# Performance work log

Measured on AMD Instinct MI355X. Metric: run time of the kernel, lower is better.

Reference implementation:

```python
import jax, jax.numpy as jnp
import numpy as np

N = 10000      # nodes
E = 160000     # edges (avg degree 16)
D = 480        # node feat dim: 128x0e+64x1e+32x2e
SH = 9         # spherical harmonics dim, lmax=2, component norm
NB = 128       # radial basis count
H = 4          # attention heads
HD = D // H    # 120 = 32x0e+16x1o+8x2e
L = 6          # transformer blocks
G = 256        # graphs in batch
MID = 480      # ffn mid dim (irreps_mlp_mid)
S = 128        # scalar (0e) channels used by the output head
FCH = 64       # radial MLP hidden (fc_neurons)
CUTOFF = 5.0
AVG_DEG = 16.0
AVG_NODES = 18.0


def _sph_l2(vec):
    # real spherical harmonics l=0,1,2 on normalized vectors, 'component' normalization
    r = jnp.linalg.norm(vec, axis=-1, keepdims=True)
    u = vec / (r + 1e-9)
    x, y, z = u[..., 0], u[..., 1], u[..., 2]
    s3, s15, s5 = jnp.sqrt(3.0), jnp.sqrt(15.0), jnp.sqrt(5.0)
    return jnp.stack([
        jnp.ones_like(x),
        s3 * x, s3 * y, s3 * z,
        s15 * x * y, s15 * y * z, 0.5 * s5 * (3.0 * z * z - 1.0),
        s15 * x * z, 0.5 * s15 * (x * x - y * y)], axis=-1)


def _rbf(d):
    centers = jnp.linspace(0.0, CUTOFF, NB)
    w = CUTOFF / NB
    return jnp.exp(-0.5 * ((d[:, None] - centers) / w) ** 2)  # [E, NB]


def _ln(x):
    mu = jnp.mean(x, axis=-1, keepdims=True)
    var = jnp.var(x, axis=-1, keepdims=True)
    return (x - mu) * jax.lax.rsqrt(var + 1e-5)


def _radial_mlp(rb, w1, w2, w3):
    h = jax.nn.silu(rb @ w1)
    h = jax.nn.silu(h @ w2)
    return h @ w3


def _segment_softmax(logits, seg, num_segments):
    m = jax.ops.segment_max(logits, seg, num_segments=num_segments)
    ex = jnp.exp(logits - m[seg])
    s = jax.ops.segment_sum(ex, seg, num_segments=num_segments)
    return ex / (s[seg] + 1e-9)


def setup_inputs():
    key = jax.random.key(0)
    ks = jax.random.split(key, 24)
    def rn(k, shape, scale):
        return jax.random.normal(k, shape, dtype=jnp.float32) * scale
    return {
        'z': jax.random.randint(ks[0], (N,), 0, 100),
        'pos': jax.random.normal(ks[1], (N, 3), dtype=jnp.float32) * 3.0,
        'batch': jnp.sort(jax.random.randint(ks[2], (N,), 0, G)),
        'edge_src': jax.random.randint(ks[3], (E,), 0, N),
        'edge_dst': jax.random.randint(ks[4], (E,), 0, N),
        'atom_emb': rn(ks[5], (100, D), 1.0),
        'W_deg_sh': rn(ks[6], (SH, D), SH ** -0.5),
        'deg_w1': rn(ks[7], (NB, FCH), NB ** -0.5),
        'deg_w2': rn(ks[8], (FCH, FCH), FCH ** -0.5),
        'deg_w3': rn(ks[9], (FCH, D), FCH ** -0.5),
        'Wv': rn(ks[10], (L, D, D), D ** -0.5),
        'Wsh': rn(ks[11], (L, SH, D), SH ** -0.5),
        'rad_w1': rn(ks[12], (L, NB, FCH), NB ** -0.5),
        'rad_w2': rn(ks[13], (L, FCH, FCH), FCH ** -0.5),
        'rad_w3': rn(ks[14], (L, FCH, D), FCH ** -0.5),
        'attn_a': rn(ks[15], (L, H, HD), HD ** -0.5),
        'Wo': rn(ks[16], (L, D, D), D ** -0.5),
        'ffn_w1': rn(ks[17], (L, D, MID), D ** -0.5),
        'ffn_w2': rn(ks[18], (L, MID, D), MID ** -0.5),
        'head_w1': rn(ks[19], (S, S), S ** -0.5),
        'head_w2': rn(ks[20], (S, S), S ** -0.5),
    }


def reference(z, pos, batch, edge_src, edge_dst, atom_emb, W_deg_sh,
              deg_w1, deg_w2, deg_w3, Wv, Wsh, rad_w1, rad_w2, rad_w3,
              attn_a, Wo, ffn_w1, ffn_w2, head_w1, head_w2):
    # edge geometry features
    vec = pos[edge_src] - pos[edge_dst]                      # [E, 3]
    sh = _sph_l2(vec)                                        # [E, SH]
    rb = _rbf(jnp.linalg.norm(vec, axis=-1))                 # [E, NB]

    # node embedding + edge-degree embedding (scatter to dst, scaled by avg degree)
    emb = atom_emb[z]                                        # [N, D]
    deg_gate = _radial_mlp(rb, deg_w1, deg_w2, deg_w3)       # [E, D]
    deg = jax.ops.segment_sum((sh @ W_deg_sh) * deg_gate, edge_dst,
                              num_segments=N) / AVG_DEG
    x = emb + deg

    # equivariant tensor-product attention blocks (gather -> per-edge TP -> segment softmax -> scatter)
    for l in range(L):
        xn = _ln(x)
        v = xn[edge_src] @ Wv[l]                             # [E, D] gather + proj
        msg = v * (sh @ Wsh[l]) * _radial_mlp(rb, rad_w1[l], rad_w2[l], rad_w3[l])
        m = msg.reshape(E, H, HD)
        logits = jnp.einsum('ehd,hd->eh', jax.nn.leaky_relu(m, 0.2), attn_a[l])
        alpha = _segment_softmax(logits, edge_dst, N)        # [E, H]
        agg = jax.ops.segment_sum(m * alpha[:, :, None], edge_dst,
                                  num_segments=N).reshape(N, D)
        x = x + agg @ Wo[l]
        x = x + jax.nn.silu(_ln(x) @ ffn_w1[l]) @ ffn_w2[l]

    # output head on scalar channels, scaled scatter over molecules
    s = _ln(x[:, :S])
    h = jax.nn.silu(s @ head_w1) @ head_w2                   # [N, S]
    out = jax.ops.segment_sum(h, batch, num_segments=G) / jnp.sqrt(AVG_NODES)
    return out
```

## Files before the change

kernel.cpp:

```cpp
#include <hip/hip_runtime.h>
#include <hip/hip_bf16.h>
#include <math.h>

#define NN 10000
#define NE 160000
#define DIM 480
#define NSH 9
#define NBASIS 128
#define NHEAD 4
#define HDIM 120
#define NL 6
#define NG 256
#define NS 128
#define FCH 64
#define CUTOFF 5.0f
#define NEB 2500

typedef __attribute__((ext_vector_type(8))) short bf8v;
typedef __attribute__((ext_vector_type(4))) float f4v;

__device__ __forceinline__ float silu_f(float v) { return v / (1.0f + __expf(-v)); }
__device__ __forceinline__ float bf2f(ushort u) { return __uint_as_float(((unsigned)u) << 16); }
__device__ __forceinline__ ushort f2bfu(float f) {
  __hip_bfloat16 h = __float2bfloat16(f);
  return *reinterpret_cast<ushort*>(&h);
}

__device__ __forceinline__ void nt_store16(char* dst, uint4 v) {
  unsigned* p = (unsigned*)dst;
  __builtin_nontemporal_store(v.x, p + 0);
  __builtin_nontemporal_store(v.y, p + 1);
  __builtin_nontemporal_store(v.z, p + 2);
  __builtin_nontemporal_store(v.w, p + 3);
}
__device__ __forceinline__ uint4 nt_load16(const char* src) {
  const unsigned* p = (const unsigned*)src;
  uint4 v;
  v.x = __builtin_nontemporal_load(p + 0);
  v.y = __builtin_nontemporal_load(p + 1);
  v.z = __builtin_nontemporal_load(p + 2);
  v.w = __builtin_nontemporal_load(p + 3);
  return v;
}

struct bf16x4 { __hip_bfloat16 v[4]; };

__global__ void k_zero_int(int* p, int n)
{
  int i = blockIdx.x * 256 + threadIdx.x;
  if (i < n) p[i] = 0;
}

__global__ void k_count(const int* __restrict__ edst, int* __restrict__ cnt)
{
  int e = blockIdx.x * 256 + threadIdx.x;
  if (e < NE) atomicAdd(&cnt[edst[e]], 1);
}

__global__ __launch_bounds__(1024)
void k_scan(const int* __restrict__ cnt, int* __restrict__ row_ptr)
{
  __shared__ int part[1024];
  int tid = threadIdx.x;
  const int per = 10;
  int base = tid * per;
  int s = 0;
  for (int i = 0; i < per; i++) { int idx = base + i; if (idx < NN) s += cnt[idx]; }
  part[tid] = s; __syncthreads();
  for (int off = 1; off < 1024; off <<= 1) {
    int v = (tid >= off) ? part[tid - off] : 0;
    __syncthreads();
    part[tid] += v;
    __syncthreads();
  }
  int run = (tid > 0) ? part[tid - 1] : 0;
  for (int i = 0; i < per; i++) {
    int idx = base + i;
    if (idx < NN) { row_ptr[idx] = run; run += cnt[idx]; }
  }
  if (tid == 1023) row_ptr[NN] = part[1023];
}

__global__ void k_fill(const int* __restrict__ edst, const int* __restrict__ row_ptr,
                       int* __restrict__ cursor, int* __restrict__ csr)
{
  int e = blockIdx.x * 256 + threadIdx.x;
  if (e >= NE) return;
  int d = edst[e];
  int p = atomicAdd(&cursor[d], 1);
  csr[row_ptr[d] + p] = e;
}

__global__ void k_geom_p(const float* __restrict__ pos, const int* __restrict__ esrc,
                         const int* __restrict__ edst, const int* __restrict__ csr,
                         __hip_bfloat16* __restrict__ shb, float* __restrict__ distp,
                         int* __restrict__ esrcp, int* __restrict__ edstp)
{
  int j = blockIdx.x * 256 + threadIdx.x;
  if (j >= NE) return;
  int e = csr[j];
  int s = esrc[e], d = edst[e];
  esrcp[j] = s;
  edstp[j] = d;
  float vx = pos[s*3+0] - pos[d*3+0];
  float vy = pos[s*3+1] - pos[d*3+1];
  float vz = pos[s*3+2] - pos[d*3+2];
  float r = sqrtf(vx*vx + vy*vy + vz*vz);
  distp[j] = r;
  float inv = 1.0f / (r + 1e-9f);
  float x = vx*inv, y = vy*inv, z = vz*inv;
  const float s3 = 1.7320508075688772f;
  const float s15 = 3.872983346207417f;
  const float s5 = 2.23606797749979f;
  float sv[9];
  sv[0] = 1.0f;
  sv[1] = s3*x; sv[2] = s3*y; sv[3] = s3*z;
  sv[4] = s15*x*y; sv[5] = s15*y*z; sv[6] = 0.5f*s5*(3.0f*z*z - 1.0f);
  sv[7] = s15*x*z; sv[8] = 0.5f*s15*(x*x - y*y);
  __hip_bfloat16* o = shb + (size_t)j * 16;
#pragma unroll
  for (int q = 0; q < 9; q++) o[q] = __float2bfloat16(sv[q]);
#pragma unroll
  for (int q = 9; q < 16; q++) o[q] = __float2bfloat16(0.f);
}

__global__ void k_prep(const float* __restrict__ deg_w3, const float* __restrict__ rad_w3,
                       const float* __restrict__ W_deg_sh, const float* __restrict__ Wsh,
                       __hip_bfloat16* __restrict__ w3T, __hip_bfloat16* __restrict__ wshT)
{
  int i = blockIdx.x * 256 + threadIdx.x;
  if (i < 7*512*64) {
    int l = i / (512*64); int r = i - l*512*64; int col = r >> 6; int k = r & 63;
    float v = 0.f;
    if (col < DIM) {
      const float* src = (l == 0) ? deg_w3 : rad_w3 + (size_t)(l-1)*FCH*DIM;
      v = src[k*DIM + col];
    }
    w3T[i] = __float2bfloat16(v);
  }
  int j = i - 7*512*64;
  if (j >= 0 && j < 7*512*32) {
    int l = j / (512*32); int r = j - l*512*32; int col = r >> 5; int q = r & 31;
    float v = 0.f;
    if (col < DIM && q < 9) {
      const float* src = (l == 0) ? W_deg_sh : Wsh + (size_t)(l-1)*NSH*DIM;
      v = src[q*DIM + col];
    }
    wshT[j] = __float2bfloat16(v);
  }
}

__global__ void k_prepw(const float* __restrict__ Wv, const float* __restrict__ Wo,
                        const float* __restrict__ f1, const float* __restrict__ f2,
                        const float* __restrict__ h1, const float* __restrict__ h2w,
                        __hip_bfloat16* __restrict__ WT)
{
  int i = blockIdx.x * 256 + threadIdx.x;
  const int big = 24*512*480;
  if (i < big) {
    int m = i / (512*480); int r = i - m*(512*480); int col = r / 480; int k = r - col*480;
    int l = m % 6; int t = m / 6;
    const float* src = (t==0 ? Wv : t==1 ? Wo : t==2 ? f1 : f2) + (size_t)l*DIM*DIM;
    float v = (col < DIM) ? src[k*DIM + col] : 0.f;
    WT[i] = __float2bfloat16(v);
  } else if (i < big + 2*128*128) {
    int j = i - big; int m = j / (128*128); int r = j - m*(128*128);
    int col = r >> 7; int k = r & 127;
    const float* src = m ? h2w : h1;
    WT[i] = __float2bfloat16(src[k*128 + col]);
  }
}

__global__ __launch_bounds__(256)
void k_radial(const float* __restrict__ dist, const float* __restrict__ w1,
              const float* __restrict__ w2, __hip_bfloat16* __restrict__ h2out)
{
  __shared__ float rbs[NBASIS][65];
  __shared__ float wsm[NBASIS * FCH];
  __shared__ float ds[64];
  int tid = threadIdx.x;
  int e0 = blockIdx.x * 64;
  if (tid < 64) ds[tid] = dist[e0 + tid];
  for (int i = tid; i < NBASIS * FCH; i += 256) wsm[i] = w1[i];
  __syncthreads();
  const float invw = (float)NBASIS / CUTOFF;
  for (int i = tid; i < NBASIS * 64; i += 256) {
    int k = i >> 6, e = i & 63;
    float c = k * (CUTOFF / 127.0f);
    float tt = (ds[e] - c) * invw;
    rbs[k][e] = __expf(-0.5f * tt * tt);
  }
  __syncthreads();
  int ty = tid >> 4, tx = tid & 15;
  float acc1[4][4] = {};
  for (int k = 0; k < NBASIS; k++) {
    float b[4];
#pragma unroll
    for (int j = 0; j < 4; j++) b[j] = wsm[k*FCH + tx*4 + j];
#pragma unroll
    for (int i = 0; i < 4; i++) {
      float a = rbs[k][ty*4 + i];
#pragma unroll
      for (int j = 0; j < 4; j++) acc1[i][j] = fmaf(a, b[j], acc1[i][j]);
    }
  }
  __syncthreads();
#pragma unroll
  for (int i = 0; i < 4; i++)
#pragma unroll
    for (int j = 0; j < 4; j++)
      rbs[tx*4 + j][ty*4 + i] = silu_f(acc1[i][j]);
  for (int i = tid; i < FCH * FCH; i += 256) wsm[i] = w2[i];
  __syncthreads();
  float acc2[4][4] = {};
  for (int k = 0; k < FCH; k++) {
    float b[4];
#pragma unroll
    for (int j = 0; j < 4; j++) b[j] = wsm[k*FCH + tx*4 + j];
#pragma unroll
    for (int i = 0; i < 4; i++) {
      float a = rbs[k][ty*4 + i];
#pragma unroll
      for (int j = 0; j < 4; j++) acc2[i][j] = fmaf(a, b[j], acc2[i][j]);
    }
  }
#pragma unroll
  for (int i = 0; i < 4; i++) {
    int e = e0 + ty*4 + i;
    bf16x4 p;
#pragma unroll
    for (int j = 0; j < 4; j++) p.v[j] = __float2bfloat16(silu_f(acc2[i][j]));
    *(bf16x4*)(h2out + (size_t)e*FCH + tx*4) = p;
  }
}

__global__ __launch_bounds__(256)
void k_stats(const float* __restrict__ in, float* __restrict__ st,
             int n, int cols, int stride)
{
  int row = blockIdx.x * 4 + (threadIdx.x >> 6);
  int lane = threadIdx.x & 63;
  if (row >= n) return;
  const float* r = in + (size_t)row * stride;
  float s = 0.f, ss = 0.f;
  for (int c = lane; c < cols; c += 64) { float v = r[c]; s += v; ss += v*v; }
  for (int off = 32; off > 0; off >>= 1) { s += __shfl_down(s, off); ss += __shfl_down(ss, off); }
  if (lane == 0) {
    float mu = s / cols;
    float var = ss / cols - mu * mu;
    st[row*2]   = mu;
    st[row*2+1] = rsqrtf(fmaxf(var, 0.f) + 1e-5f);
  }
}

template<int ADD, int SILU, int LNA, int OBF16>
__global__ __launch_bounds__(256)
void k_gemmm(const float* __restrict__ A, const __hip_bfloat16* __restrict__ BT,
             float* __restrict__ C, __hip_bfloat16* __restrict__ Cb,
             const float* __restrict__ st, int M, int K, int Nc, int lda)
{
  __shared__ __align__(16) char smA[4096];
  __shared__ __align__(16) char smB[8192];
  __shared__ float smu[64], srs[64];
  int tid = threadIdx.x;
  int lane = tid & 63;
  int wv = tid >> 6;
  int l15 = lane & 15, l4 = lane >> 4;
  int row0 = blockIdx.x * 64;
  int col0 = blockIdx.y * 128;
  if (LNA && tid < 64) {
    int gr = row0 + tid;
    float m2 = 0.f, r2 = 1.f;
    if (gr < M) { m2 = st[gr*2]; r2 = st[gr*2+1]; }
    smu[tid] = m2; srs[tid] = r2;
  }
  f4v z4 = {0.f,0.f,0.f,0.f};
  f4v acc[8];
#pragma unroll
  for (int ct = 0; ct < 8; ct++) acc[ct] = z4;

  int arow = tid >> 2, aq = tid & 3;
  int bcol = tid >> 1, bh = tid & 1;
  for (int k0 = 0; k0 < K; k0 += 32) {
    __syncthreads();
    {
      int grow = row0 + arow;
      float f[8];
      if (grow < M) {
        const float* ap = A + (size_t)grow * lda + k0 + aq*8;
        float4 v0 = *(const float4*)ap;
        float4 v1 = *(const float4*)(ap + 4);
        f[0]=v0.x; f[1]=v0.y; f[2]=v0.z; f[3]=v0.w;
        f[4]=v1.x; f[5]=v1.y; f[6]=v1.z; f[7]=v1.w;
      } else {
#pragma unroll
        for (int q = 0; q < 8; q++) f[q] = 0.f;
      }
      if (LNA) {
        float mu = smu[arow], rs = srs[arow];
#pragma unroll
        for (int q = 0; q < 8; q++) f[q] = (f[q] - mu) * rs;
      }
      unsigned u[4];
#pragma unroll
      for (int q = 0; q < 4; q++)
        u[q] = (unsigned)f2bfu(f[2*q]) | ((unsigned)f2bfu(f[2*q+1]) << 16);
      int base = arow*64 + aq*16;
      *(uint4*)(smA + (base ^ ((arow&7)<<4))) = make_uint4(u[0],u[1],u[2],u[3]);
    }
    {
      const ushort* bp = (const ushort*)BT + (size_t)(col0 + bcol) * K + k0 + bh*16;
      uint4 v0 = *(const uint4*)bp;
      uint4 v1 = *(const uint4*)(bp + 8);
      int base = bcol*64 + bh*32;
      *(uint4*)(smB + (base ^ ((bcol&7)<<4))) = v0;
      *(uint4*)(smB + ((base+16) ^ ((bcol&7)<<4))) = v1;
    }
    __syncthreads();
    int r0 = wv*16 + l15;
    bf8v a0 = *(const bf8v*)(smA + ((r0*64 + l4*16) ^ ((r0&7)<<4)));
#pragma unroll
    for (int ct = 0; ct < 8; ct++) {
      int cc = ct*16 + l15;
      bf8v b = *(const bf8v*)(smB + ((cc*64 + l4*16) ^ ((cc&7)<<4)));
      acc[ct] = __builtin_amdgcn_mfma_f32_16x16x32_bf16(a0, b, acc[ct], 0, 0, 0);
    }
  }
#pragma unroll
  for (int ct = 0; ct < 8; ct++)
#pragma unroll
  for (int e = 0; e < 4; e++) {
    int row = row0 + wv*16 + l4*4 + e;
    int col = col0 + ct*16 + l15;
    if (row < M && col < Nc) {
      float v = acc[ct][e];
      if (SILU) v = silu_f(v);
      if (OBF16) Cb[(size_t)row * Nc + col] = __float2bfloat16(v);
      else {
        float* p = C + (size_t)row * Nc + col;
        if (ADD) *p += v; else *p = v;
      }
    }
  }
}

template<int MODE, int STOREM>
__global__ __launch_bounds__(256)
void k_msgm(const __hip_bfloat16* __restrict__ h2, const __hip_bfloat16* __restrict__ shb,
            const int* __restrict__ esrcp, const int* __restrict__ edstp,
            const __hip_bfloat16* __restrict__ w3T, const __hip_bfloat16* __restrict__ wshT,
            const float* __restrict__ aa, const __hip_bfloat16* __restrict__ y,
            const float* __restrict__ alpha, float* __restrict__ outbuf,
            float* __restrict__ logits, __hip_bfloat16* __restrict__ msgb)
{
  __shared__ __align__(16) char sm_h2[8192];
  __shared__ __align__(16) char sm_w3[16384];
  __shared__ __align__(16) char sm_sh[4096];
  __shared__ __align__(16) char sm_wsh[8192];
  __shared__ int srcs[(MODE<=1)?64:1];
  __shared__ int dsts[(MODE>=1)?64:1];
  __shared__ int segidL[(MODE>=1)?64:1];
  __shared__ int seg_dstL[(MODE>=1)?32:1];

  int bid = blockIdx.x;
  int xcd = bid & 7;
  const int qq = NEB >> 3, rr = NEB & 7;
  int basee = (xcd < rr) ? xcd * (qq + 1) : rr * (qq + 1) + (xcd - rr) * qq;
  int eblk = basee + (bid >> 3);
  int e0 = eblk * 64;

  int tid = threadIdx.x;
  int lane = tid & 63;
  int wv = tid >> 6;
  int l15 = lane & 15, l4 = lane >> 4;
  int wrow0 = wv * 16;

  for (int c = tid; c < 512; c += 256) {
    int r = c >> 3, s = c & 7;
    uint4 v = *(const uint4*)((const char*)h2 + (size_t)(e0 + r) * 128 + s * 16);
    *(uint4*)(sm_h2 + ((r * 128 + s * 16) ^ ((r & 7) << 4))) = v;
  }
  {
    int r = tid >> 2, q = tid & 3;
    uint4 v = make_uint4(0u, 0u, 0u, 0u);
    if (q < 2)
      v = *(const uint4*)((const ushort*)shb + (size_t)(e0 + r) * 16 + q * 8);
    *(uint4*)(sm_sh + ((r * 64 + q * 16) ^ ((r & 7) << 4))) = v;
  }
  if (tid < 64) {
    if (MODE <= 1) srcs[tid] = esrcp[e0 + tid];
    if (MODE >= 1) dsts[tid] = edstp[e0 + tid];
  }
  __syncthreads();

  int nseg = 0;
  if (MODE >= 1) {
    if (tid < 64) {
      bool flag = (tid == 0) || (dsts[tid] != dsts[tid - 1]);
      unsigned long long m = __ballot(flag ? 1 : 0);
      unsigned long long below = m & (~0ull >> (63 - tid));
      int sg = __popcll(below) - 1;
      segidL[tid] = sg;
      if (flag && sg < 32) seg_dstL[sg] = dsts[tid];
    }
    __syncthreads();
    nseg = segidL[63] + 1;
  }

  int srcs4[4];
  float4 al4[4];
#pragma unroll
  for (int e = 0; e < 4; e++) {
    int rl = wrow0 + l4 * 4 + e;
    if (MODE <= 1) srcs4[e] = srcs[rl];
    if (MODE == 1) al4[e] = *(const float4*)(alpha + (size_t)(e0 + rl) * 4);
  }

  const ushort* yus = (const ushort*)y;
  f4v z4 = {0.f, 0.f, 0.f, 0.f};
  float lacc[4][4];
  if (MODE == 0) {
#pragma unroll
    for (int e = 0; e < 4; e++)
#pragma unroll
      for (int h = 0; h < 4; h++) lacc[e][h] = 0.f;
  }

#pragma unroll
  for (int ci = 0; ci < 4; ci++) {
    int col0 = ci * 128;
    __syncthreads();
    for (int c = tid; c < 1024; c += 256) {
      int r = c >> 3, s = c & 7;
      uint4 v = *(const uint4*)((const char*)w3T + (size_t)(col0 + r) * 128 + s * 16);
      *(uint4*)(sm_w3 + ((r * 128 + s * 16) ^ ((r & 7) << 4))) = v;
    }
    for (int c = tid; c < 512; c += 256) {
      int r = c >> 2, q = c & 3;
      uint4 v = *(const uint4*)((const ushort*)wshT + (size_t)(col0 + r) * 32 + q * 8);
      *(uint4*)(sm_wsh + ((r * 64 + q * 16) ^ ((r & 7) << 4))) = v;
    }
    __syncthreads();

    f4v g[8];
#pragma unroll
    for (int ct = 0; ct < 8; ct++) g[ct] = z4;

#pragma unroll
    for (int ks = 0; ks < 2; ks++) {
      int k0b = (ks * 32 + l4 * 8) * 2;
      int r0 = wrow0 + l15;
      bf8v a0 = *(const bf8v*)(sm_h2 + ((r0 * 128 + k0b) ^ ((r0 & 7) << 4)));
#pragma unroll
      for (int ct = 0; ct < 8; ct++) {
        int cc = ct * 16 + l15;
        bf8v b = *(const bf8v*)(sm_w3 + ((cc * 128 + k0b) ^ ((cc & 7) << 4)));
        g[ct] = __builtin_amdgcn_mfma_f32_16x16x32_bf16(a0, b, g[ct], 0, 0, 0);
      }
    }

    {
      int r0 = wrow0 + l15;
      bf8v shA = *(const bf8v*)(sm_sh + ((r0 * 64 + l4 * 16) ^ ((r0 & 7) << 4)));
#pragma unroll
      for (int ct = 0; ct < 8; ct++) {
        int cc = ct * 16 + l15;
        int col = col0 + cc;
        bf8v wB = *(const bf8v*)(sm_wsh + ((cc * 64 + l4 * 16) ^ ((cc & 7) << 4)));
        f4v sw4 = __builtin_amdgcn_mfma_f32_16x16x32_bf16(shA, wB, z4, 0, 0, 0);
#pragma unroll
        for (int e = 0; e < 4; e++) {
          float yv;
          if (MODE == 2) yv = 1.f;
          else yv = (col < DIM) ? bf2f(yus[(size_t)srcs4[e] * DIM + col]) : 0.f;
          float mv = yv * sw4[e] * g[ct][e];
          if (MODE == 1) {
            float av = (col < 120) ? al4[e].x : (col < 240) ? al4[e].y
                     : (col < 360) ? al4[e].z : al4[e].w;
            mv *= av;
          }
          if (MODE == 2) mv *= (1.0f / 16.0f);
          g[ct][e] = mv;
        }
      }
    }

    if (MODE == 0) {
      float aav[8];
#pragma unroll
      for (int ct = 0; ct < 8; ct++) {
        int col = col0 + ct * 16 + l15;
        aav[ct] = (col < DIM) ? aa[col] : 0.f;
      }
#pragma unroll
      for (int e = 0; e < 4; e++) {
        float sA = 0.f, sB = 0.f;
#pragma unroll
        for (int ct = 0; ct < 8; ct++) {
          int col = col0 + ct * 16 + l15;
          float mv = g[ct][e];
          float lv = (mv > 0.f) ? mv : 0.2f * mv;
          float c = lv * aav[ct];
          if (col / 120 == ci) sA += c; else sB += c;
        }
#pragma unroll
        for (int off = 1; off < 16; off <<= 1) {
          sA += __shfl_xor(sA, off, 16);
          sB += __shfl_xor(sB, off, 16);
        }
        lacc[e][ci] += sA;
        if (ci < 3) lacc[e][ci + 1] += sB;
      }
      if (STOREM) {
        __syncthreads();
#pragma unroll
        for (int ct = 0; ct < 8; ct++) {
          int cc = ct * 16 + l15;
          int ebase = wrow0 + l4 * 4;
          ushort4 pk;
          pk.x = f2bfu(g[ct][0]); pk.y = f2bfu(g[ct][1]);
          pk.z = f2bfu(g[ct][2]); pk.w = f2bfu(g[ct][3]);
          *(ushort4*)(sm_w3 + ((cc * 128 + ebase * 2) ^ ((cc & 7) << 4))) = pk;
        }
        __syncthreads();
        char* gdst = (char*)msgb + (size_t)(eblk * 4 + ci) * 16384;
#pragma unroll
        for (int k = 0; k < 4; k++) {
          int o = tid * 16 + k * 4096;
          uint4 v = *(const uint4*)(sm_w3 + o);
          nt_store16(gdst + o, v);
        }
      }
    } else if (nseg > 32) {
#pragma unroll
      for (int e = 0; e < 4; e++) {
        int rl = wrow0 + l4 * 4 + e;
        int dd = dsts[rl];
#pragma unroll
        for (int ct = 0; ct < 8; ct++) {
          int col = col0 + ct * 16 + l15;
          if (col < DIM) atomicAdd(&outbuf[(size_t)dd * DIM + col], g[ct][e]);
        }
      }
    } else {
      __syncthreads();
#pragma unroll
      for (int ct = 0; ct < 8; ct++) {
        int cc = ct * 16 + l15;
        int ebase = wrow0 + l4 * 4;
        ushort4 pk;
        pk.x = f2bfu(g[ct][0]); pk.y = f2bfu(g[ct][1]);
        pk.z = f2bfu(g[ct][2]); pk.w = f2bfu(g[ct][3]);
        *(ushort4*)(sm_w3 + ((cc * 128 + ebase * 2) ^ ((cc & 7) << 4))) = pk;
      }
      __syncthreads();
      f4v p[2][2];
      p[0][0] = z4; p[0][1] = z4; p[1][0] = z4; p[1][1] = z4;
#pragma unroll
      for (int ks = 0; ks < 2; ks++) {
        int k0 = ks * 32 + l4 * 8;
        bf8v a0, a1;
#pragma unroll
        for (int e2 = 0; e2 < 8; e2++) {
          int sg = segidL[k0 + e2];
          a0[e2] = (sg == l15)      ? (short)0x3F80 : (short)0;
          a1[e2] = (sg == l15 + 16) ? (short)0x3F80 : (short)0;
        }
#pragma unroll
        for (int c2 = 0; c2 < 2; c2++) {
          int cc = (wv * 2 + c2) * 16 + l15;
          bf8v bm = *(const bf8v*)(sm_w3 + ((cc * 128 + k0 * 2) ^ ((cc & 7) << 4)));
          p[0][c2] = __builtin_amdgcn_mfma_f32_16x16x32_bf16(a0, bm, p[0][c2], 0, 0, 0);
          p[1][c2] = __builtin_amdgcn_mfma_f32_16x16x32_bf16(a1, bm, p[1][c2], 0, 0, 0);
        }
      }
#pragma unroll
      for (int rt = 0; rt < 2; rt++)
#pragma unroll
      for (int c2 = 0; c2 < 2; c2++)
#pragma unroll
      for (int e = 0; e < 4; e++) {
        int seg = rt * 16 + l4 * 4 + e;
        int col = col0 + (wv * 2 + c2) * 16 + l15;
        if (seg < nseg && col < DIM) {
          float v = p[rt][c2][e];
          float* ptr = outbuf + (size_t)seg_dstL[seg] * DIM + col;
          if (seg == 0 || seg == nseg - 1) atomicAdd(ptr, v);
          else if (MODE == 1) *ptr = v;
          else *ptr += v;
        }
      }
    }
  }

  if (MODE == 0) {
#pragma unroll
    for (int e = 0; e < 4; e++) {
      int row = e0 + wrow0 + l4 * 4 + e;
      if (l15 == 0) {
        logits[(size_t)row * 4 + 0] = lacc[e][0];
        logits[(size_t)row * 4 + 1] = lacc[e][1];
        logits[(size_t)row * 4 + 2] = lacc[e][2];
        logits[(size_t)row * 4 + 3] = lacc[e][3];
      }
    }
  }
}

__global__ __launch_bounds__(256)
void k_aggm(const __hip_bfloat16* __restrict__ msgb, const int* __restrict__ edstp,
            const float* __restrict__ alpha, float* __restrict__ agg)
{
  __shared__ __align__(16) char smM[16384];
  __shared__ __align__(16) float alsq[64][4];
  __shared__ int dsts[64];
  __shared__ int segidL[64];
  __shared__ int seg_dstL[32];

  int bid = blockIdx.x;
  int swzb = (bid & 7) * 1250 + (bid >> 3);
  int e0   = (swzb >> 2) * 64;
  int col0 = (swzb & 3) * 128;
  int tid = threadIdx.x;
  int lane = tid & 63;
  int wv = tid >> 6;
  int l15 = lane & 15, l4 = lane >> 4;

  if (tid < 64) {
    dsts[tid] = edstp[e0 + tid];
    *(float4*)&alsq[tid][0] = *(const float4*)(alpha + (size_t)(e0 + tid) * 4);
  }
  __syncthreads();

  int nseg = 0;
  if (tid < 64) {
    bool flag = (tid == 0) || (dsts[tid] != dsts[tid - 1]);
    unsigned long long m = __ballot(flag ? 1 : 0);
    unsigned long long below = m & (~0ull >> (63 - tid));
    int sg = __popcll(below) - 1;
    segidL[tid] = sg;
    if (flag && sg < 32) seg_dstL[sg] = dsts[tid];
  }
  __syncthreads();
  nseg = segidL[63] + 1;

  const char* gsrc = (const char*)msgb + (size_t)swzb * 16384;
  uint4 vv[4];
#pragma unroll
  for (int k = 0; k < 4; k++) {
    int o = tid * 16 + k * 4096;
    uint4 v = nt_load16(gsrc + o);
    int cc = o >> 7;
    int col = col0 + cc;
    int h = (col < DIM) ? (col / 120) : 3;
    int be = ((o & 127) ^ ((cc & 7) << 4)) >> 1;
    unsigned w[4] = {v.x, v.y, v.z, v.w};
#pragma unroll
    for (int q = 0; q < 4; q++) {
      float lo = bf2f((ushort)(w[q] & 0xffffu)) * alsq[be + 2*q][h];
      float hi = bf2f((ushort)(w[q] >> 16))     * alsq[be + 2*q + 1][h];
      w[q] = (unsigned)f2bfu(lo) | ((unsigned)f2bfu(hi) << 16);
    }
    vv[k] = make_uint4(w[0], w[1], w[2], w[3]);
    *(uint4*)(smM + o) = vv[k];
  }
  __syncthreads();

  if (nseg > 32) {
#pragma unroll
    for (int k = 0; k < 4; k++) {
      int o = tid * 16 + k * 4096;
      int cc = o >> 7;
      int col = col0 + cc;
      if (col >= DIM) continue;
      int be = ((o & 127) ^ ((cc & 7) << 4)) >> 1;
      unsigned w[4] = {vv[k].x, vv[k].y, vv[k].z, vv[k].w};
#pragma unroll
      for (int q = 0; q < 4; q++) {
        atomicAdd(&agg[(size_t)dsts[be + 2*q]   * DIM + col], bf2f((ushort)(w[q] & 0xffffu)));
        atomicAdd(&agg[(size_t)dsts[be + 2*q+1] * DIM + col], bf2f((ushort)(w[q] >> 16)));
      }
    }
    return;
  }

  f4v z4 = {0.f,0.f,0.f,0.f};
  f4v p[2][2];
  p[0][0] = z4; p[0][1] = z4; p[1][0] = z4; p[1][1] = z4;
#pragma unroll
  for (int ks = 0; ks < 2; ks++) {
    int k0 = ks * 32 + l4 * 8;
    bf8v a0, a1;
#pragma unroll
    for (int e2 = 0; e2 < 8; e2++) {
      int sg = segidL[k0 + e2];
      a0[e2] = (sg == l15)      ? (short)0x3F80 : (short)0;
      a1[e2] = (sg == l15 + 16) ? (short)0x3F80 : (short)0;
    }
#pragma unroll
    for (int c2 = 0; c2 < 2; c2++) {
      int cc = (wv * 2 + c2) * 16 + l15;
      bf8v bm = *(const bf8v*)(smM + ((cc * 128 + k0 * 2) ^ ((cc & 7) << 4)));
      p[0][c2] = __builtin_amdgcn_mfma_f32_16x16x32_bf16(a0, bm, p[0][c2], 0, 0, 0);
      p[1][c2] = __builtin_amdgcn_mfma_f32_16x16x32_bf16(a1, bm, p[1][c2], 0, 0, 0);
    }
  }
#pragma unroll
  for (int rt = 0; rt < 2; rt++)
#pragma unroll
  for (int c2 = 0; c2 < 2; c2++)
#pragma unroll
  for (int e = 0; e < 4; e++) {
    int seg = rt * 16 + l4 * 4 + e;
    int col = col0 + (wv * 2 + c2) * 16 + l15;
    if (seg < nseg && col < DIM) {
      float v = p[rt][c2][e];
      float* ptr = agg + (size_t)seg_dstL[seg] * DIM + col;
      if (seg == 0 || seg == nseg - 1) atomicAdd(ptr, v);
      else *ptr = v;
    }
  }
}

__global__ void k_alpha(const int* __restrict__ row_ptr, const float* __restrict__ logits,
                        float* __restrict__ alpha)
{
  int i = blockIdx.x * 256 + threadIdx.x;
  if (i >= NN * NHEAD) return;
  int d = i >> 2, h = i & 3;
  int beg = row_ptr[d], end = row_ptr[d+1];
  if (beg == end) return;
  float m = -1e30f;
  for (int j = beg; j < end; j++) m = fmaxf(m, logits[(size_t)j*NHEAD + h]);
  float s = 0.f;
  for (int j = beg; j < end; j++) {
    float ex = __expf(logits[(size_t)j*NHEAD + h] - m);
    alpha[(size_t)j*NHEAD + h] = ex;
    s += ex;
  }
  float inv = 1.f / (s + 1e-9f);
  for (int j = beg; j < end; j++) alpha[(size_t)j*NHEAD + h] *= inv;
}

__global__ void k_init_x(const int* __restrict__ z, const float* __restrict__ emb,
                         float* __restrict__ x)
{
  int i = blockIdx.x * 256 + threadIdx.x;
  if (i >= NN * DIM) return;
  int n = i / DIM, c = i - n * DIM;
  x[i] = emb[(size_t)z[n]*DIM + c];
}

__global__ void k_scatter(const float* __restrict__ h, const int* __restrict__ batch,
                          float* __restrict__ out)
{
  int i = blockIdx.x * 256 + threadIdx.x;
  if (i >= NN * NS) return;
  int n = i >> 7;
  atomicAdd(&out[(size_t)batch[n]*NS + (i & 127)], h[i] * 0.23570226039551584f);
}

extern "C" void kernel_launch(void* const* d_in, const int* in_sizes, int n_in,
                              void* d_out, int out_size, void* d_ws, size_t ws_size,
                              hipStream_t stream)
{
  const int*   z        = (const int*)  d_in[0];
  const float* pos      = (const float*)d_in[1];
  const int*   batch    = (const int*)  d_in[2];
  const int*   esrc     = (const int*)  d_in[3];
  const int*   edst     = (const int*)  d_in[4];
  const float* atom_emb = (const float*)d_in[5];
  const float* W_deg_sh = (const float*)d_in[6];
  const float* deg_w1   = (const float*)d_in[7];
  const float* deg_w2   = (const float*)d_in[8];
  const float* deg_w3   = (const float*)d_in[9];
  const float* Wv       = (const float*)d_in[10];
  const float* Wsh      = (const float*)d_in[11];
  const float* rad_w1   = (const float*)d_in[12];
  const float* rad_w2   = (const float*)d_in[13];
  const float* rad_w3   = (const float*)d_in[14];
  const float* attn_a   = (const float*)d_in[15];
  const float* Wo       = (const float*)d_in[16];
  const float* ffn_w1   = (const float*)d_in[17];
  const float* ffn_w2   = (const float*)d_in[18];
  const float* head_w1  = (const float*)d_in[19];
  const float* head_w2  = (const float*)d_in[20];
  float* out = (float*)d_out;

  float* x      = (float*)d_ws;
  float* statsb = x      + (size_t)NN * DIM;
  float* agg    = statsb + (size_t)NN * 2;
  float* distp  = agg    + (size_t)NN * DIM;
  float* logitsb= distp  + (size_t)NE;
  float* alphab = logitsb+ (size_t)NE * NHEAD * 2;
  __hip_bfloat16* yb    = (__hip_bfloat16*)(alphab + (size_t)NE * NHEAD);
  __hip_bfloat16* h2b   = yb + (size_t)NN * DIM;
  __hip_bfloat16* shb16 = h2b + (size_t)NE * FCH;
  __hip_bfloat16* w3Tb  = shb16 + (size_t)NE * 16;
  __hip_bfloat16* wshTb = w3Tb + (size_t)7 * 512 * 64;
  __hip_bfloat16* bigWT = wshTb + (size_t)7 * 512 * 32;
  int* cnt      = (int*)(bigWT + (size_t)24*512*480 + 2*128*128);
  int* row_ptr  = cnt + NN;
  int* csr      = row_ptr + NN + 1;
  int* cursor   = csr + NE;
  int* esrcp    = cursor + NN;
  int* edstp    = esrcp + NE;
  __hip_bfloat16* msgb = (__hip_bfloat16*)(edstp + NE);
  float* tmp = logitsb;

  size_t needed = (size_t)((char*)msgb + (size_t)10000 * 16384 - (char*)d_ws);
  bool fast = ws_size >= needed;

  dim3 b256(256);
  k_zero_int<<<(NN+255)/256, b256, 0, stream>>>(cnt, NN);
  k_count<<<(NE+255)/256, b256, 0, stream>>>(edst, cnt);
  k_scan<<<1, 1024, 0, stream>>>(cnt, row_ptr);
  k_zero_int<<<(NN+255)/256, b256, 0, stream>>>(cursor, NN);
  k_fill<<<(NE+255)/256, b256, 0, stream>>>(edst, row_ptr, cursor, csr);
  k_geom_p<<<(NE+255)/256, b256, 0, stream>>>(pos, esrc, edst, csr, shb16, distp, esrcp, edstp);
  k_prep<<<(7*512*64 + 7*512*32 + 255)/256, b256, 0, stream>>>(deg_w3, rad_w3, W_deg_sh, Wsh,
      w3Tb, wshTb);
  k_prepw<<<(24*512*480 + 2*128*128 + 255)/256, b256, 0, stream>>>(Wv, Wo, ffn_w1, ffn_w2,
      head_w1, head_w2, bigWT);

  k_radial<<<NE/64, b256, 0, stream>>>(distp, deg_w1, deg_w2, h2b);
  k_init_x<<<(NN*DIM+255)/256, b256, 0, stream>>>(z, atom_emb, x);
  k_msgm<2,0><<<NEB, b256, 0, stream>>>(h2b, shb16, esrcp, edstp, w3Tb, wshTb,
      nullptr, nullptr, nullptr, x, nullptr, nullptr);

  dim3 gemm_grid(157, 4);
  dim3 head_grid(157, 1);
  for (int l = 0; l < NL; l++) {
    const float* w1_l  = rad_w1 + (size_t)l*NBASIS*FCH;
    const float* w2_l  = rad_w2 + (size_t)l*FCH*FCH;
    const float* aa_l  = attn_a + (size_t)l*NHEAD*HDIM;
    const __hip_bfloat16* w3T_l  = w3Tb  + (size_t)(l+1)*512*64;
    const __hip_bfloat16* wshT_l = wshTb + (size_t)(l+1)*512*32;
    const __hip_bfloat16* WvT_l = bigWT + (size_t)(0+l)*512*480;
    const __hip_bfloat16* WoT_l = bigWT + (size_t)(6+l)*512*480;
    const __hip_bfloat16* F1T_l = bigWT + (size_t)(12+l)*512*480;
    const __hip_bfloat16* F2T_l = bigWT + (size_t)(18+l)*512*480;

    k_stats<<<(NN+3)/4, b256, 0, stream>>>(x, statsb, NN, DIM, DIM);
    k_gemmm<0,0,1,1><<<gemm_grid, b256, 0, stream>>>(x, WvT_l, nullptr, yb, statsb,
        NN, DIM, DIM, DIM);
    k_radial<<<NE/64, b256, 0, stream>>>(distp, w1_l, w2_l, h2b);
    if (fast) {
      k_msgm<0,1><<<NEB, b256, 0, stream>>>(h2b, shb16, esrcp, edstp, w3T_l, wshT_l,
          aa_l, yb, nullptr, nullptr, logitsb, msgb);
      k_alpha<<<(NN*NHEAD+255)/256, b256, 0, stream>>>(row_ptr, logitsb, alphab);
      hipMemsetAsync(agg, 0, (size_t)NN * DIM * sizeof(float), stream);
      k_aggm<<<10000, b256, 0, stream>>>(msgb, edstp, alphab, agg);
    } else {
      k_msgm<0,0><<<NEB, b256, 0, stream>>>(h2b, shb16, esrcp, edstp, w3T_l, wshT_l,
          aa_l, yb, nullptr, nullptr, logitsb, nullptr);
      k_alpha<<<(NN*NHEAD+255)/256, b256, 0, stream>>>(row_ptr, logitsb, alphab);
      hipMemsetAsync(agg, 0, (size_t)NN * DIM * sizeof(float), stream);
      k_msgm<1,0><<<NEB, b256, 0, stream>>>(h2b, shb16, esrcp, edstp, w3T_l, wshT_l,
          nullptr, yb, alphab, agg, nullptr, nullptr);
    }
    k_gemmm<1,0,0,0><<<gemm_grid, b256, 0, stream>>>(agg, WoT_l, x, nullptr, nullptr,
        NN, DIM, DIM, DIM);
    k_stats<<<(NN+3)/4, b256, 0, stream>>>(x, statsb, NN, DIM, DIM);
    k_gemmm<0,1,1,0><<<gemm_grid, b256, 0, stream>>>(x, F1T_l, agg, nullptr, statsb,
        NN, DIM, DIM, DIM);
    k_gemmm<1,0,0,0><<<gemm_grid, b256, 0, stream>>>(agg, F2T_l, x, nullptr, nullptr,
        NN, DIM, DIM, DIM);
  }

  const __hip_bfloat16* H1T = bigWT + (size_t)24*512*480;
  const __hip_bfloat16* H2T = H1T + 128*128;
  k_stats<<<(NN+3)/4, b256, 0, stream>>>(x, statsb, NN, NS, DIM);
  k_gemmm<0,1,1,0><<<head_grid, b256, 0, stream>>>(x, H1T, agg, nullptr, statsb,
      NN, NS, NS, DIM);
  k_gemmm<0,0,0,0><<<head_grid, b256, 0, stream>>>(agg, H2T, tmp, nullptr, nullptr,
      NN, NS, NS, NS);
  hipMemsetAsync(d_out, 0, (size_t)NG * NS * sizeof(float), stream);
  k_scatter<<<(NN*NS+255)/256, b256, 0, stream>>>(tmp, batch, out);
}
```

Measured before the change: 2.377 ms.

## Fuse layernorm stats into residual GEMM epilogue and loop aggm over column tiles

The residual-add GEMMs now accumulate per-row sum and sum-of-squares via shuffles and atomics into a stats buffer, and a tiny finalize kernel replaces the separate k_stats pass that reread x. The aggregation kernel now processes all four column tiles of an edge block in one workgroup (2500 blocks instead of 10000) with a balanced XCD mapping, reusing destination/segment setup and alpha loads. This adds atomics and extra memsets per layer, and single-pass variance in fp32 with atomic ordering may change numerics slightly.

```diff
diff --git a/kernel.cpp b/kernel.cpp
--- a/kernel.cpp
+++ b/kernel.cpp
@@ -253,11 +253,23 @@
   }
 }
 
-template<int ADD, int SILU, int LNA, int OBF16>
+__global__ void k_finstat(const float* __restrict__ stacc, float* __restrict__ st, int n)
+{
+  int row = blockIdx.x * 256 + threadIdx.x;
+  if (row >= n) return;
+  float s = stacc[row*2], ss = stacc[row*2+1];
+  float mu = s / DIM;
+  float var = ss / DIM - mu * mu;
+  st[row*2]   = mu;
+  st[row*2+1] = rsqrtf(fmaxf(var, 0.f) + 1e-5f);
+}
+
+template<int ADD, int SILU, int LNA, int OBF16, int STATS>
 __global__ __launch_bounds__(256)
 void k_gemmm(const float* __restrict__ A, const __hip_bfloat16* __restrict__ BT,
              float* __restrict__ C, __hip_bfloat16* __restrict__ Cb,
-             const float* __restrict__ st, int M, int K, int Nc, int lda)
+             const float* __restrict__ st, int M, int K, int Nc, int lda,
+             float* __restrict__ stacc)
 {
   __shared__ __align__(16) char smA[4096];
   __shared__ __align__(16) char smB[8192];
@@ -327,18 +339,33 @@
     }
   }
 #pragma unroll
-  for (int ct = 0; ct < 8; ct++)
-#pragma unroll
   for (int e = 0; e < 4; e++) {
     int row = row0 + wv*16 + l4*4 + e;
-    int col = col0 + ct*16 + l15;
-    if (row < M && col < Nc) {
-      float v = acc[ct][e];
-      if (SILU) v = silu_f(v);
-      if (OBF16) Cb[(size_t)row * Nc + col] = __float2bfloat16(v);
-      else {
-        float* p = C + (size_t)row * Nc + col;
-        if (ADD) *p += v; else *p = v;
+    float s = 0.f, ss = 0.f;
+#pragma unroll
+    for (int ct = 0; ct < 8; ct++) {
+      int col = col0 + ct*16 + l15;
+      if (row < M && col < Nc) {
+        float v = acc[ct][e];
+        if (SILU) v = silu_f(v);
+        if (OBF16) Cb[(size_t)row * Nc + col] = __float2bfloat16(v);
+        else {
+          float* p = C + (size_t)row * Nc + col;
+          float xn = ADD ? (*p + v) : v;
+          *p = xn;
+          if (STATS) { s += xn; ss += xn * xn; }
+        }
+      }
+    }
+    if (STATS) {
+#pragma unroll
+      for (int off = 1; off < 16; off <<= 1) {
+        s  += __shfl_xor(s,  off, 16);
+        ss += __shfl_xor(ss, off, 16);
+      }
+      if (l15 == 0 && row < M) {
+        atomicAdd(&stacc[row*2],   s);
+        atomicAdd(&stacc[row*2+1], ss);
       }
     }
   }
@@ -618,9 +645,12 @@
   __shared__ int seg_dstL[32];
 
   int bid = blockIdx.x;
-  int swzb = (bid & 7) * 1250 + (bid >> 3);
-  int e0   = (swzb >> 2) * 64;
-  int col0 = (swzb & 3) * 128;
+  int xcd = bid & 7;
+  const int qq = NEB >> 3, rr = NEB & 7;
+  int basee = (xcd < rr) ? xcd * (qq + 1) : rr * (qq + 1) + (xcd - rr) * qq;
+  int eblk = basee + (bid >> 3);
+  int e0 = eblk * 64;
+
   int tid = threadIdx.x;
   int lane = tid & 63;
   int wv = tid >> 6;
@@ -644,80 +674,85 @@
   __syncthreads();
   nseg = segidL[63] + 1;
 
-  const char* gsrc = (const char*)msgb + (size_t)swzb * 16384;
-  uint4 vv[4];
-#pragma unroll
-  for (int k = 0; k < 4; k++) {
-    int o = tid * 16 + k * 4096;
-    uint4 v = nt_load16(gsrc + o);
-    int cc = o >> 7;
-    int col = col0 + cc;
-    int h = (col < DIM) ? (col / 120) : 3;
-    int be = ((o & 127) ^ ((cc & 7) << 4)) >> 1;
-    unsigned w[4] = {v.x, v.y, v.z, v.w};
-#pragma unroll
-    for (int q = 0; q < 4; q++) {
-      float lo = bf2f((ushort)(w[q] & 0xffffu)) * alsq[be + 2*q][h];
-      float hi = bf2f((ushort)(w[q] >> 16))     * alsq[be + 2*q + 1][h];
-      w[q] = (unsigned)f2bfu(lo) | ((unsigned)f2bfu(hi) << 16);
-    }
-    vv[k] = make_uint4(w[0], w[1], w[2], w[3]);
-    *(uint4*)(smM + o) = vv[k];
-  }
-  __syncthreads();
-
-  if (nseg > 32) {
+  f4v z4 = {0.f,0.f,0.f,0.f};
+#pragma unroll
+  for (int ci = 0; ci < 4; ci++) {
+    int col0 = ci * 128;
+    __syncthreads();
+    const char* gsrc = (const char*)msgb + (size_t)(eblk * 4 + ci) * 16384;
+    uint4 vv[4];
 #pragma unroll
     for (int k = 0; k < 4; k++) {
       int o = tid * 16 + k * 4096;
+      uint4 v = nt_load16(gsrc + o);
       int cc = o >> 7;
       int col = col0 + cc;
-      if (col >= DIM) continue;
+      int h = (col < DIM) ? (col / 120) : 3;
       int be = ((o & 127) ^ ((cc & 7) << 4)) >> 1;
-      unsigned w[4] = {vv[k].x, vv[k].y, vv[k].z, vv[k].w};
+      unsigned w[4] = {v.x, v.y, v.z, v.w};
 #pragma unroll
       for (int q = 0; q < 4; q++) {
-        atomicAdd(&agg[(size_t)dsts[be + 2*q]   * DIM + col], bf2f((ushort)(w[q] & 0xffffu)));
-        atomicAdd(&agg[(size_t)dsts[be + 2*q+1] * DIM + col], bf2f((ushort)(w[q] >> 16)));
-      }
-    }
-    return;
-  }
-
-  f4v z4 = {0.f,0.f,0.f,0.f};
-  f4v p[2][2];
-  p[0][0] = z4; p[0][1] = z4; p[1][0] = z4; p[1][1] = z4;
-#pragma unroll
-  for (int ks = 0; ks < 2; ks++) {
-    int k0 = ks * 32 + l4 * 8;
-    bf8v a0, a1;
-#pragma unroll
-    for (int e2 = 0; e2 < 8; e2++) {
-      int sg = segidL[k0 + e2];
-      a0[e2] = (sg == l15)      ? (short)0x3F80 : (short)0;
-      a1[e2] = (sg == l15 + 16) ? (short)0x3F80 : (short)0;
-    }
-#pragma unroll
-    for (int c2 = 0; c2 < 2; c2++) {
-      int cc = (wv * 2 + c2) * 16 + l15;
-      bf8v bm = *(const bf8v*)(smM + ((cc * 128 + k0 * 2) ^ ((cc & 7) << 4)));
-      p[0][c2] = __builtin_amdgcn_mfma_f32_16x16x32_bf16(a0, bm, p[0][c2], 0, 0, 0);
-      p[1][c2] = __builtin_amdgcn_mfma_f32_16x16x32_bf16(a1, bm, p[1][c2], 0, 0, 0);
-    }
-  }
-#pragma unroll
-  for (int rt = 0; rt < 2; rt++)
-#pragma unroll
-  for (int c2 = 0; c2 < 2; c2++)
-#pragma unroll
-  for (int e = 0; e < 4; e++) {
-    int seg = rt * 16 + l4 * 4 + e;
-    int col = col0 + (wv * 2 + c2) * 16 + l15;
-    if (seg < nseg && col < DIM) {
-      float v = p[rt][c2][e];
-      float* ptr = agg + (size_t)seg_dstL[seg] * DIM + col;
-      if (seg == 0 || seg == nseg - 1) atomicAdd(ptr, v);
-      else *ptr = v;
+        float lo = bf2f((ushort)(w[q] & 0xffffu)) * alsq[be + 2*q][h];
+        float hi = bf2f((ushort)(w[q] >> 16))     * alsq[be + 2*q + 1][h];
+        w[q] = (unsigned)f2bfu(lo) | ((unsigned)f2bfu(hi) << 16);
+      }
+      vv[k] = make_uint4(w[0], w[1], w[2], w[3]);
+      *(uint4*)(smM + o) = vv[k];
+    }
+    __syncthreads();
+
+    if (nseg > 32) {
+#pragma unroll
+      for (int k = 0; k < 4; k++) {
+        int o = tid * 16 + k * 4096;
+        int cc = o >> 7;
+        int col = col0 + cc;
+        if (col >= DIM) continue;
+        int be = ((o & 127) ^ ((cc & 7) << 4)) >> 1;
+        unsigned w[4] = {vv[k].x, vv[k].y, vv[k].z, vv[k].w};
+#pragma unroll
+        for (int q = 0; q < 4; q++) {
+          atomicAdd(&agg[(size_t)dsts[be + 2*q]   * DIM + col], bf2f((ushort)(w[q] & 0xffffu)));
+          atomicAdd(&agg[(size_t)dsts[be + 2*q+1] * DIM + col], bf2f((ushort)(w[q] >> 16)));
+        }
+      }
+      continue;
+    }
+
+    f4v p[2][2];
+    p[0][0] = z4; p[0][1] = z4; p[1][0] = z4; p[1][1] = z4;
+#pragma unroll
+    for (int ks = 0; ks < 2; ks++) {
+      int k0 = ks * 32 + l4 * 8;
+      bf8v a0, a1;
+#pragma unroll
+      for (int e2 = 0; e2 < 8; e2++) {
+        int sg = segidL[k0 + e2];
+        a0[e2] = (sg == l15)      ? (short)0x3F80 : (short)0;
+        a1[e2] = (sg == l15 + 16) ? (short)0x3F80 : (short)0;
+      }
+#pragma unroll
+      for (int c2 = 0; c2 < 2; c2++) {
+        int cc = (wv * 2 + c2) * 16 + l15;
+        bf8v bm = *(const bf8v*)(smM + ((cc * 128 + k0 * 2) ^ ((cc & 7) << 4)));
+        p[0][c2] = __builtin_amdgcn_mfma_f32_16x16x32_bf16(a0, bm, p[0][c2], 0, 0, 0);
+        p[1][c2] = __builtin_amdgcn_mfma_f32_16x16x32_bf16(a1, bm, p[1][c2], 0, 0, 0);
+      }
+    }
+#pragma unroll
+    for (int rt = 0; rt < 2; rt++)
+#pragma unroll
+    for (int c2 = 0; c2 < 2; c2++)
+#pragma unroll
+    for (int e = 0; e < 4; e++) {
+      int seg = rt * 16 + l4 * 4 + e;
+      int col = col0 + (wv * 2 + c2) * 16 + l15;
+      if (seg < nseg && col < DIM) {
+        float v = p[rt][c2][e];
+        float* ptr = agg + (size_t)seg_dstL[seg] * DIM + col;
+        if (seg == 0 || seg == nseg - 1) atomicAdd(ptr, v);
+        else *ptr = v;
+      }
     }
   }
 }
@@ -789,7 +824,8 @@
 
   float* x      = (float*)d_ws;
   float* statsb = x      + (size_t)NN * DIM;
-  float* agg    = statsb + (size_t)NN * 2;
+  float* stacc  = statsb + (size_t)NN * 2;
+  float* agg    = stacc  + (size_t)NN * 2;
   float* distp  = agg    + (size_t)NN * DIM;
   float* logitsb= distp  + (size_t)NE;
   float* alphab = logitsb+ (size_t)NE * NHEAD * 2;
@@ -827,6 +863,7 @@
   k_init_x<<<(NN*DIM+255)/256, b256, 0, stream>>>(z, atom_emb, x);
   k_msgm<2,0><<<NEB, b256, 0, stream>>>(h2b, shb16, esrcp, edstp, w3Tb, wshTb,
       nullptr, nullptr, nullptr, x, nullptr, nullptr);
+  k_stats<<<(NN+3)/4, b256, 0, stream>>>(x, statsb, NN, DIM, DIM);
 
   dim3 gemm_grid(157, 4);
   dim3 head_grid(157, 1);
@@ -841,16 +878,15 @@
     const __hip_bfloat16* F1T_l = bigWT + (size_t)(12+l)*512*480;
     const __hip_bfloat16* F2T_l = bigWT + (size_t)(18+l)*512*480;
 
-    k_stats<<<(NN+3)/4, b256, 0, stream>>>(x, statsb, NN, DIM, DIM);
-    k_gemmm<0,0,1,1><<<gemm_grid, b256, 0, stream>>>(x, WvT_l, nullptr, yb, statsb,
-        NN, DIM, DIM, DIM);
+    k_gemmm<0,0,1,1,0><<<gemm_grid, b256, 0, stream>>>(x, WvT_l, nullptr, yb, statsb,
+        NN, DIM, DIM, DIM, nullptr);
     k_radial<<<NE/64, b256, 0, stream>>>(distp, w1_l, w2_l, h2b);
     if (fast) {
       k_msgm<0,1><<<NEB, b256, 0, stream>>>(h2b, shb16, esrcp, edstp, w3T_l, wshT_l,
           aa_l, yb, nullptr, nullptr, logitsb, msgb);
       k_alpha<<<(NN*NHEAD+255)/256, b256, 0, stream>>>(row_ptr, logitsb, alphab);
       hipMemsetAsync(agg, 0, (size_t)NN * DIM * sizeof(float), stream);
-      k_aggm<<<10000, b256, 0, stream>>>(msgb, edstp, alphab, agg);
+      k_aggm<<<NEB, b256, 0, stream>>>(msgb, edstp, alphab, agg);
     } else {
       k_msgm<0,0><<<NEB, b256, 0, stream>>>(h2b, shb16, esrcp, edstp, w3T_l, wshT_l,
           aa_l, yb, nullptr, nullptr, logitsb, nullptr);
@@ -859,22 +895,25 @@
       k_msgm<1,0><<<NEB, b256, 0, stream>>>(h2b, shb16, esrcp, edstp, w3T_l, wshT_l,
           nullptr, yb, alphab, agg, nullptr, nullptr);
     }
-    k_gemmm<1,0,0,0><<<gemm_grid, b256, 0, stream>>>(agg, WoT_l, x, nullptr, nullptr,
-        NN, DIM, DIM, DIM);
-    k_stats<<<(NN+3)/4, b256, 0, stream>>>(x, statsb, NN, DIM, DIM);
-    k_gemmm<0,1,1,0><<<gemm_grid, b256, 0, stream>>>(x, F1T_l, agg, nullptr, statsb,
-        NN, DIM, DIM, DIM);
-    k_gemmm<1,0,0,0><<<gemm_grid, b256, 0, stream>>>(agg, F2T_l, x, nullptr, nullptr,
-        NN, DIM, DIM, DIM);
+    hipMemsetAsync(stacc, 0, (size_t)NN * 2 * sizeof(float), stream);
+    k_gemmm<1,0,0,0,1><<<gemm_grid, b256, 0, stream>>>(agg, WoT_l, x, nullptr, nullptr,
+        NN, DIM, DIM, DIM, stacc);
+    k_finstat<<<(NN+255)/256, b256, 0, stream>>>(stacc, statsb, NN);
+    k_gemmm<0,1,1,0,0><<<gemm_grid, b256, 0, stream>>>(x, F1T_l, agg, nullptr, statsb,
+        NN, DIM, DIM, DIM, nullptr);
+    hipMemsetAsync(stacc, 0, (size_t)NN * 2 * sizeof(float), stream);
+    k_gemmm<1,0,0,0,1><<<gemm_grid, b256, 0, stream>>>(agg, F2T_l, x, nullptr, nullptr,
+        NN, DIM, DIM, DIM, stacc);
+    k_finstat<<<(NN+255)/256, b256, 0, stream>>>(stacc, statsb, NN);
   }
 
   const __hip_bfloat16* H1T = bigWT + (size_t)24*512*480;
   const __hip_bfloat16* H2T = H1T + 128*128;
   k_stats<<<(NN+3)/4, b256, 0, stream>>>(x, statsb, NN, NS, DIM);
-  k_gemmm<0,1,1,0><<<head_grid, b256, 0, stream>>>(x, H1T, agg, nullptr, statsb,
-      NN, NS, NS, DIM);
-  k_gemmm<0,0,0,0><<<head_grid, b256, 0, stream>>>(agg, H2T, tmp, nullptr, nullptr,
-      NN, NS, NS, NS);
+  k_gemmm<0,1,1,0,0><<<head_grid, b256, 0, stream>>>(x, H1T, agg, nullptr, statsb,
+      NN, NS, NS, DIM, nullptr);
+  k_gemmm<0,0,0,0,0><<<head_grid, b256, 0, stream>>>(agg, H2T, tmp, nullptr, nullptr,
+      NN, NS, NS, NS, nullptr);
   hipMemsetAsync(d_out, 0, (size_t)NG * NS * sizeof(float), stream);
   k_scatter<<<(NN*NS+255)/256, b256, 0, stream>>>(tmp, batch, out);
 }
```

After: 2.396 ms. Within noise of the previous version (+0.8%).
